# Optimization experiments

Measured on AMD Instinct MI355X. Metric: run time of the kernel, lower is better.

The kernel has to match this reference:

```python
import jax, jax.numpy as jnp
import numpy as np

T, B, I, H = 512, 256, 256, 256


def setup_inputs() -> dict:
    key = jax.random.key(0)
    ks = jax.random.split(key, 7)
    sk = 1.0 / np.sqrt(H)
    u = lambda k, shape: jax.random.uniform(k, shape, jnp.float32, -sk, sk)
    return {
        "x": jax.random.normal(ks[0], (T, B, I), jnp.float32),
        "W_ih": u(ks[1], (3 * H, I)),   # rows ordered [r, z, n] as in torch GRUCell
        "W_hh": u(ks[2], (3 * H, H)),
        "b_ih": u(ks[3], (3 * H,)),
        "b_hh": u(ks[4], (3 * H,)),
        "W_out": u(ks[5], (1, H)),
        "b_out": u(ks[6], (1,)),
    }


def _gru_forward(x, W_ih, W_hh, b_ih, b_hh):
    # Precompute input projections for all timesteps in one big GEMM: [T,B,3H]
    gi_all = jnp.einsum("tbi,gi->tbg", x, W_ih) + b_ih

    def step(h, gi):
        gh = h @ W_hh.T + b_hh                      # [B, 3H]
        i_r, i_z, i_n = jnp.split(gi, 3, axis=-1)
        h_r, h_z, h_n = jnp.split(gh, 3, axis=-1)
        r = jax.nn.sigmoid(i_r + h_r)
        z = jax.nn.sigmoid(i_z + h_z)
        n = jnp.tanh(i_n + r * h_n)
        h_new = (1.0 - z) * n + z * h
        return h_new, None

    h0 = jnp.zeros((x.shape[1], W_hh.shape[1]), x.dtype)
    h_final, _ = jax.lax.scan(step, h0, gi_all)
    return h_final


def reference(x, W_ih, W_hh, b_ih, b_hh, W_out, b_out):
    h = _gru_forward(x, W_ih, W_hh, b_ih, b_hh)
    return jax.nn.sigmoid(h @ W_out.T + b_out)      # [B, 1]
```

## Files before the change

### kernel.cpp

```cpp
#include <hip/hip_runtime.h>
#include <hip/hip_bf16.h>


#define TT 512
#define BB 256
#define II 256
#define HH 256

#define SRZ (-1.4426950408889634f)
#define SN  (2.8853900817779268f)

typedef __attribute__((ext_vector_type(8))) short short8;
typedef __attribute__((ext_vector_type(4))) float f32x4;

__device__ __forceinline__ unsigned short rne_bf16(float f) {
  union { float f; unsigned u; } v; v.f = f;
  unsigned r = v.u + 0x7FFFu + ((v.u >> 16) & 1u);
  return (unsigned short)(r >> 16);
}
__device__ __forceinline__ float bf2f(unsigned short b) {
  union { unsigned u; float f; } v; v.u = ((unsigned)b) << 16;
  return v.f;
}
__device__ __forceinline__ float blo(unsigned p) {
  union { unsigned u; float f; } v; v.u = p << 16; return v.f;
}
__device__ __forceinline__ float bhi(unsigned p) {
  union { unsigned u; float f; } v; v.u = p & 0xffff0000u; return v.f;
}
__device__ __forceinline__ float sigm(float x) { return 1.0f / (1.0f + __expf(-x)); }
__device__ __forceinline__ float tanhfast(float x) {
  return 1.0f - 2.0f / (__expf(2.0f * x) + 1.0f);
}

__device__ __forceinline__ short8 ldw8(const float* __restrict__ p) {
  float4 a = *reinterpret_cast<const float4*>(p);
  float4 b = *reinterpret_cast<const float4*>(p + 4);
  short8 r;
  r[0] = (short)rne_bf16(a.x); r[1] = (short)rne_bf16(a.y);
  r[2] = (short)rne_bf16(a.z); r[3] = (short)rne_bf16(a.w);
  r[4] = (short)rne_bf16(b.x); r[5] = (short)rne_bf16(b.y);
  r[6] = (short)rne_bf16(b.z); r[7] = (short)rne_bf16(b.w);
  return r;
}
__device__ __forceinline__ short8 ldw8s(const float* __restrict__ p, float s) {
  float4 a = *reinterpret_cast<const float4*>(p);
  float4 b = *reinterpret_cast<const float4*>(p + 4);
  short8 r;
  r[0] = (short)rne_bf16(a.x * s); r[1] = (short)rne_bf16(a.y * s);
  r[2] = (short)rne_bf16(a.z * s); r[3] = (short)rne_bf16(a.w * s);
  r[4] = (short)rne_bf16(b.x * s); r[5] = (short)rne_bf16(b.y * s);
  r[6] = (short)rne_bf16(b.z * s); r[7] = (short)rne_bf16(b.w * s);
  return r;
}

#define SWZ8(m, k) ((m) * 256 + ((k) ^ (((m) & 7) * 8)))
#define SWZ(m, k) ((m) * 256 + ((k) ^ ((m) * 16)))

__device__ __forceinline__ void pin_agpr(short8& w) {
  asm volatile("" : "+a"(w));
}
__device__ __forceinline__ void mfma_ag(f32x4& d, short8 a, const short8& b) {
  asm volatile("v_mfma_f32_16x16x32_bf16 %0, %1, %2, %0"
               : "+v"(d) : "v"(a), "a"(b));
}
__device__ __forceinline__ void mfma_ag_f(f32x4& d, short8 a, const short8& b) {
  asm volatile("s_nop 1\n\tv_mfma_f32_16x16x32_bf16 %0, %1, %2, %0"
               : "+v"(d) : "v"(a), "a"(b));
}
__device__ __forceinline__ void mfma_v(f32x4& d, short8 a, short8 b) {
  asm volatile("v_mfma_f32_16x16x32_bf16 %0, %1, %2, %0"
               : "+v"(d) : "v"(a), "v"(b));
}
__device__ __forceinline__ void mfma_v_f(f32x4& d, short8 a, short8 b) {
  asm volatile("s_nop 1\n\tv_mfma_f32_16x16x32_bf16 %0, %1, %2, %0"
               : "+v"(d) : "v"(a), "v"(b));
}
__device__ __forceinline__ void mfma_fence6(f32x4& a0, f32x4& a1, f32x4& a2,
                                            f32x4& a3, f32x4& a4, f32x4& a5) {
  asm volatile("s_nop 7\n\ts_nop 7"
               : "+v"(a0), "+v"(a1), "+v"(a2), "+v"(a3), "+v"(a4), "+v"(a5));
}
__device__ __forceinline__ unsigned cvtpk_bf16(float lo, float hi) {
  unsigned r;
  asm("v_cvt_pk_bf16_f32 %0, %1, %2" : "=v"(r) : "v"(lo), "v"(hi));
  return r;
}

__global__ __launch_bounds__(512)
__attribute__((amdgpu_waves_per_eu(2, 2)))
void gi_gemm8(const float* __restrict__ x, const float* __restrict__ Wih,
              const float* __restrict__ bih, const float* __restrict__ bhh,
              unsigned short* __restrict__ gi, int ntiles) {
  __shared__ __align__(16) unsigned short ax[2][4096];
  const int tid = threadIdx.x, l = tid & 63, w = tid >> 6;
  const int g4 = l >> 4, i15 = l & 15;

  short8 wf[3][2][8];
  float bs[3][2];
#pragma unroll
  for (int g = 0; g < 3; ++g)
#pragma unroll
    for (int ct = 0; ct < 2; ++ct) {
      int j = 32 * w + 16 * ct + i15;
      float s = (g == 2) ? SN : SRZ;
#pragma unroll
      for (int c = 0; c < 8; ++c)
        wf[g][ct][c] = ldw8s(Wih + (size_t)(g * 256 + j) * 256 + c * 32 + g4 * 8, s);
      bs[g][ct] = (g == 2) ? SN * bih[512 + j]
                           : SRZ * (bih[g * 256 + j] + bhh[g * 256 + j]);
    }

  auto stage = [&](int buf, int t) {
#pragma unroll
    for (int p = 0; p < 2; ++p) {
      int idx = p * 512 + tid;
      int m = idx >> 6, k0 = (idx & 63) << 2;
      float4 v = *reinterpret_cast<const float4*>(x + (size_t)t * 4096 + m * 256 + k0);
      ushort4 b;
      b.x = rne_bf16(v.x); b.y = rne_bf16(v.y);
      b.z = rne_bf16(v.z); b.w = rne_bf16(v.w);
      *reinterpret_cast<ushort4*>(&ax[buf][SWZ8(m, k0)]) = b;
    }
  };

  if (blockIdx.x >= ntiles) return;
  stage(0, blockIdx.x);
  int cur = 0;
  for (int tile = blockIdx.x; tile < ntiles; tile += 256) {
    __syncthreads();
    int tn = tile + 256;
    if (tn < ntiles) stage(cur ^ 1, tn);
    f32x4 aR[2] = {{0, 0, 0, 0}, {0, 0, 0, 0}};
    f32x4 aZ[2] = {{0, 0, 0, 0}, {0, 0, 0, 0}};
    f32x4 aN[2] = {{0, 0, 0, 0}, {0, 0, 0, 0}};
#pragma unroll
    for (int c = 0; c < 8; ++c) {
      short8 ah = *reinterpret_cast<const short8*>(&ax[cur][SWZ8(l & 15, c * 32 + g4 * 8)]);
#pragma unroll
      for (int ct = 0; ct < 2; ++ct) {
        if (c == 0) {
          mfma_v_f(aR[ct], ah, wf[0][ct][0]);
          mfma_v_f(aZ[ct], ah, wf[1][ct][0]);
          mfma_v_f(aN[ct], ah, wf[2][ct][0]);
        } else {
          mfma_v(aR[ct], ah, wf[0][ct][c]);
          mfma_v(aZ[ct], ah, wf[1][ct][c]);
          mfma_v(aN[ct], ah, wf[2][ct][c]);
        }
      }
    }
    mfma_fence6(aR[0], aR[1], aZ[0], aZ[1], aN[0], aN[1]);
    unsigned short* gp = gi + ((size_t)tile * 512 + (size_t)(w * 64 + l)) * 24;
    short8 oR, oZ, oN;
#pragma unroll
    for (int ct = 0; ct < 2; ++ct)
#pragma unroll
      for (int q = 0; q < 4; ++q) {
        oR[ct * 4 + q] = (short)rne_bf16(aR[ct][q] + bs[0][ct]);
        oZ[ct * 4 + q] = (short)rne_bf16(aZ[ct][q] + bs[1][ct]);
        oN[ct * 4 + q] = (short)rne_bf16(aN[ct][q] + bs[2][ct]);
      }
    *reinterpret_cast<short8*>(gp) = oR;
    *reinterpret_cast<short8*>(gp + 8) = oZ;
    *reinterpret_cast<short8*>(gp + 16) = oN;
    cur ^= 1;
  }
}

__global__ __launch_bounds__(512)
__attribute__((amdgpu_waves_per_eu(2, 2)))
void gru_step10(const float* __restrict__ Whh, const float* __restrict__ bhh,
                const float* __restrict__ Wout, const float* __restrict__ bout,
                const unsigned short* __restrict__ gi, float* __restrict__ hchk,
                float* __restrict__ out, int t0, int nt) {
  __shared__ __align__(16) unsigned char arena[147456];
  unsigned short* ldsn = (unsigned short*)arena;
  unsigned short* hbuf0 = (unsigned short*)(arena + 131072);
  unsigned short* hbuf1 = (unsigned short*)(arena + 139264);
  const int tid = threadIdx.x, l = tid & 63, w = tid >> 6;
  const int g4 = l >> 4, i15 = l & 15;
  const int bx = blockIdx.x, b0 = bx * 16;

  short8 wR[2][8], wZ[2][8];
#pragma unroll
  for (int ct = 0; ct < 2; ++ct) {
    int j = 32 * w + 16 * ct + i15;
#pragma unroll
    for (int c = 0; c < 8; ++c) {
      wR[ct][c] = ldw8s(Whh + (size_t)j * 256 + c * 32 + g4 * 8, SRZ);
      wZ[ct][c] = ldw8s(Whh + (size_t)(256 + j) * 256 + c * 32 + g4 * 8, SRZ);
      pin_agpr(wR[ct][c]);
      pin_agpr(wZ[ct][c]);
    }
  }
  asm volatile("s_nop 7\n\ts_nop 7" ::: "memory");

  float cn[2];
#pragma unroll
  for (int tl = 0; tl < 2; ++tl) {
    int j = 32 * w + 16 * tl + i15;
#pragma unroll
    for (int c = 0; c < 8; ++c) {
      short8 fn = ldw8s(Whh + (size_t)(512 + j) * 256 + c * 32 + g4 * 8, SN);
      *reinterpret_cast<short8*>(
          &ldsn[(size_t)(((w * 2 + tl) * 8 + c) * 64 + l) * 8]) = fn;
    }
    cn[tl] = SN * bhh[512 + j];
  }
  const unsigned short* nbase = ldsn + (size_t)l * 8 + (size_t)w * 8192;

  unsigned hp[2][2];
  if (t0 == 0) {
    hp[0][0] = hp[0][1] = hp[1][0] = hp[1][1] = 0;
    for (int i = tid; i < 4096; i += 512) hbuf0[i] = 0;
  } else {
#pragma unroll
    for (int ct = 0; ct < 2; ++ct) {
      int j = 32 * w + 16 * ct + i15;
      float v0 = hchk[(size_t)(b0 + 4 * g4 + 0) * 256 + j];
      float v1 = hchk[(size_t)(b0 + 4 * g4 + 1) * 256 + j];
      float v2 = hchk[(size_t)(b0 + 4 * g4 + 2) * 256 + j];
      float v3 = hchk[(size_t)(b0 + 4 * g4 + 3) * 256 + j];
      hp[ct][0] = cvtpk_bf16(v0, v1);
      hp[ct][1] = cvtpk_bf16(v2, v3);
      hbuf0[SWZ8(4 * g4 + 0, j)] = (unsigned short)hp[ct][0];
      hbuf0[SWZ8(4 * g4 + 1, j)] = (unsigned short)(hp[ct][0] >> 16);
      hbuf0[SWZ8(4 * g4 + 2, j)] = (unsigned short)hp[ct][1];
      hbuf0[SWZ8(4 * g4 + 3, j)] = (unsigned short)(hp[ct][1] >> 16);
    }
  }
  const unsigned short* gp = gi + ((size_t)(bx * 8 + w) * 64 + l) * 24;
  __syncthreads();

#pragma unroll 1
  for (int lt = 0; lt < nt; ++lt) {
    short8 gR = *reinterpret_cast<const short8*>(gp);
    short8 gZ = *reinterpret_cast<const short8*>(gp + 8);
    short8 gN = *reinterpret_cast<const short8*>(gp + 16);

    f32x4 aR[2] = {{0, 0, 0, 0}, {0, 0, 0, 0}};
    f32x4 aZ[2] = {{0, 0, 0, 0}, {0, 0, 0, 0}};
    f32x4 aN[2] = {{0, 0, 0, 0}, {0, 0, 0, 0}};
    const unsigned short* hb = (lt & 1) ? hbuf1 : hbuf0;
    unsigned short* hw = (lt & 1) ? hbuf0 : hbuf1;
#pragma unroll
    for (int c = 0; c < 8; ++c) {
      short8 ah = *reinterpret_cast<const short8*>(&hb[SWZ8(l & 15, c * 32 + g4 * 8)]);
      short8 fn0 = *reinterpret_cast<const short8*>(nbase + c * 512);
      short8 fn1 = *reinterpret_cast<const short8*>(nbase + (8 + c) * 512);
      if (c == 0) {
        mfma_ag_f(aR[0], ah, wR[0][0]);
        mfma_ag_f(aR[1], ah, wR[1][0]);
        mfma_ag_f(aZ[0], ah, wZ[0][0]);
        mfma_ag_f(aZ[1], ah, wZ[1][0]);
        mfma_v_f(aN[0], ah, fn0);
        mfma_v_f(aN[1], ah, fn1);
      } else {
        mfma_ag(aR[0], ah, wR[0][c]);
        mfma_ag(aR[1], ah, wR[1][c]);
        mfma_ag(aZ[0], ah, wZ[0][c]);
        mfma_ag(aZ[1], ah, wZ[1][c]);
        mfma_v(aN[0], ah, fn0);
        mfma_v(aN[1], ah, fn1);
      }
    }
    mfma_fence6(aR[0], aR[1], aZ[0], aZ[1], aN[0], aN[1]);

#pragma unroll
    for (int ct = 0; ct < 2; ++ct) {
      int j = 32 * w + 16 * ct + i15;
      float hq[4];
#pragma unroll
      for (int q = 0; q < 4; ++q) {
        float hold = (q & 1) ? bhi(hp[ct][q >> 1]) : blo(hp[ct][q >> 1]);
        float rr = __builtin_amdgcn_rcpf(
            1.0f + __builtin_amdgcn_exp2f(aR[ct][q] + bf2f((unsigned short)gR[ct * 4 + q])));
        float zz = __builtin_amdgcn_rcpf(
            1.0f + __builtin_amdgcn_exp2f(aZ[ct][q] + bf2f((unsigned short)gZ[ct * 4 + q])));
        float y = bf2f((unsigned short)gN[ct * 4 + q]) + rr * (aN[ct][q] + cn[ct]);
        float nn = 1.0f - 2.0f * __builtin_amdgcn_rcpf(1.0f + __builtin_amdgcn_exp2f(y));
        hq[q] = nn + zz * (hold - nn);
      }
      hp[ct][0] = cvtpk_bf16(hq[0], hq[1]);
      hp[ct][1] = cvtpk_bf16(hq[2], hq[3]);
      hw[SWZ8(4 * g4 + 0, j)] = (unsigned short)hp[ct][0];
      hw[SWZ8(4 * g4 + 1, j)] = (unsigned short)(hp[ct][0] >> 16);
      hw[SWZ8(4 * g4 + 2, j)] = (unsigned short)hp[ct][1];
      hw[SWZ8(4 * g4 + 3, j)] = (unsigned short)(hp[ct][1] >> 16);
    }
    gp += 196608;
    __syncthreads();
  }

  if (t0 + nt < TT) {
#pragma unroll
    for (int ct = 0; ct < 2; ++ct) {
      int j = 32 * w + 16 * ct + i15;
      hchk[(size_t)(b0 + 4 * g4 + 0) * 256 + j] = blo(hp[ct][0]);
      hchk[(size_t)(b0 + 4 * g4 + 1) * 256 + j] = bhi(hp[ct][0]);
      hchk[(size_t)(b0 + 4 * g4 + 2) * 256 + j] = blo(hp[ct][1]);
      hchk[(size_t)(b0 + 4 * g4 + 3) * 256 + j] = bhi(hp[ct][1]);
    }
  } else {
    float* hfin = (float*)arena;
#pragma unroll
    for (int ct = 0; ct < 2; ++ct) {
      int j = 32 * w + 16 * ct + i15;
      hfin[(4 * g4 + 0) * 256 + j] = blo(hp[ct][0]);
      hfin[(4 * g4 + 1) * 256 + j] = bhi(hp[ct][0]);
      hfin[(4 * g4 + 2) * 256 + j] = blo(hp[ct][1]);
      hfin[(4 * g4 + 3) * 256 + j] = bhi(hp[ct][1]);
    }
    __syncthreads();
#pragma unroll
    for (int rr = 0; rr < 2; ++rr) {
      int r = 2 * w + rr;
      float s = 0.0f;
#pragma unroll
      for (int k = 0; k < 4; ++k) {
        int col = l + 64 * k;
        s += hfin[r * 256 + col] * Wout[col];
      }
#pragma unroll
      for (int off = 32; off > 0; off >>= 1) s += __shfl_xor(s, off, 64);
      if (l == 0) out[b0 + r] = sigm(s + bout[0]);
    }
  }
}

__global__ __launch_bounds__(1024, 1) void gru_fused_legacy(
    const float* __restrict__ x, const float* __restrict__ Wih,
    const float* __restrict__ Whh, const float* __restrict__ bih,
    const float* __restrict__ bhh, const float* __restrict__ Wout,
    const float* __restrict__ bout, float* __restrict__ out) {
  __shared__ unsigned short hbuf[2][16 * 256];
  __shared__ unsigned short xbuf[2][16 * 256];
  __shared__ float hfin[16][256];
  int tid = threadIdx.x, lane = tid & 63, w = tid >> 6;
  int i15 = lane & 15, g4 = lane >> 4;
  int b0 = blockIdx.x * 16;
  int j = 16 * w + i15;

  short8 whh0[8], whh1[8], whh2[8], wih0[8], wih1[8], wih2[8];
#pragma unroll
  for (int c = 0; c < 8; ++c) {
    int ko = c * 32 + g4 * 8;
    whh0[c] = ldw8(Whh + (size_t)j * 256 + ko);
    whh1[c] = ldw8(Whh + (size_t)(256 + j) * 256 + ko);
    whh2[c] = ldw8(Whh + (size_t)(512 + j) * 256 + ko);
    wih0[c] = ldw8(Wih + (size_t)j * 256 + ko);
    wih1[c] = ldw8(Wih + (size_t)(256 + j) * 256 + ko);
    wih2[c] = ldw8(Wih + (size_t)(512 + j) * 256 + ko);
  }
  float bias_r = bih[j] + bhh[j];
  float bias_z = bih[256 + j] + bhh[256 + j];
  float bihn = bih[512 + j], bhhn = bhh[512 + j];

  f32x4 h = {0, 0, 0, 0};
  for (int idx = tid; idx < 16 * 256; idx += 1024) hbuf[0][idx] = 0;
  {
    int m = tid >> 6, k0 = (tid & 63) << 2;
    float4 v = *reinterpret_cast<const float4*>(x + (size_t)b0 * II + m * 256 + k0);
    ushort4 b;
    b.x = rne_bf16(v.x); b.y = rne_bf16(v.y);
    b.z = rne_bf16(v.z); b.w = rne_bf16(v.w);
    *reinterpret_cast<ushort4*>(&xbuf[0][SWZ(m, k0)]) = b;
  }
  __syncthreads();

  for (int lt = 0; lt < TT; ++lt) {
    int cur = lt & 1, nxt = cur ^ 1;
    short8 ah[8], axf[8];
#pragma unroll
    for (int c = 0; c < 8; ++c) {
      int m = lane & 15, k0 = c * 32 + g4 * 8;
      ah[c] = *reinterpret_cast<const short8*>(&hbuf[cur][SWZ(m, k0)]);
      axf[c] = *reinterpret_cast<const short8*>(&xbuf[cur][SWZ(m, k0)]);
    }
    f32x4 gr = {0, 0, 0, 0}, gz = {0, 0, 0, 0}, gn = {0, 0, 0, 0};
    f32x4 ar = {0, 0, 0, 0}, az = {0, 0, 0, 0}, an = {0, 0, 0, 0};
#pragma unroll
    for (int c = 0; c < 8; ++c) {
      gr = __builtin_amdgcn_mfma_f32_16x16x32_bf16(axf[c], wih0[c], gr, 0, 0, 0);
      gz = __builtin_amdgcn_mfma_f32_16x16x32_bf16(axf[c], wih1[c], gz, 0, 0, 0);
      gn = __builtin_amdgcn_mfma_f32_16x16x32_bf16(axf[c], wih2[c], gn, 0, 0, 0);
    }
    if (lt + 1 < TT) {
      int m = tid >> 6, k0 = (tid & 63) << 2;
      float4 v = *reinterpret_cast<const float4*>(
          x + ((size_t)(lt + 1) * BB + b0) * II + m * 256 + k0);
      ushort4 b;
      b.x = rne_bf16(v.x); b.y = rne_bf16(v.y);
      b.z = rne_bf16(v.z); b.w = rne_bf16(v.w);
      *reinterpret_cast<ushort4*>(&xbuf[nxt][SWZ(m, k0)]) = b;
    }
#pragma unroll
    for (int c = 0; c < 8; ++c) {
      ar = __builtin_amdgcn_mfma_f32_16x16x32_bf16(ah[c], whh0[c], ar, 0, 0, 0);
      az = __builtin_amdgcn_mfma_f32_16x16x32_bf16(ah[c], whh1[c], az, 0, 0, 0);
      an = __builtin_amdgcn_mfma_f32_16x16x32_bf16(ah[c], whh2[c], an, 0, 0, 0);
    }
#pragma unroll
    for (int q = 0; q < 4; ++q) {
      float r = sigm(ar[q] + gr[q] + bias_r);
      float zz = sigm(az[q] + gz[q] + bias_z);
      float nn = tanhfast(gn[q] + bihn + r * (an[q] + bhhn));
      float hq = (1.0f - zz) * nn + zz * h[q];
      h[q] = hq;
      hbuf[nxt][SWZ(g4 * 4 + q, j)] = rne_bf16(hq);
    }
    __syncthreads();
  }
#pragma unroll
  for (int q = 0; q < 4; ++q) hfin[g4 * 4 + q][j] = h[q];
  __syncthreads();
  float s = 0.0f;
#pragma unroll
  for (int i = 0; i < 4; ++i) {
    int k = lane + 64 * i;
    s += hfin[w][k] * Wout[k];
  }
#pragma unroll
  for (int off = 32; off > 0; off >>= 1) s += __shfl_xor(s, off, 64);
  if (lane == 0) out[b0 + w] = sigm(s + bout[0]);
}

extern "C" void kernel_launch(void* const* d_in, const int* in_sizes, int n_in,
                              void* d_out, int out_size, void* d_ws, size_t ws_size,
                              hipStream_t stream) {
  const float* x    = (const float*)d_in[0];
  const float* Wih  = (const float*)d_in[1];
  const float* Whh  = (const float*)d_in[2];
  const float* bih  = (const float*)d_in[3];
  const float* bhh  = (const float*)d_in[4];
  const float* Wout = (const float*)d_in[5];
  const float* bout = (const float*)d_in[6];
  float* out = (float*)d_out;

  const size_t HBYTES = (size_t)BB * HH * sizeof(float);
  const size_t STEP_BYTES = (size_t)16 * 512 * 48;
  size_t gi_cap = ws_size > HBYTES ? ws_size - HBYTES : 0;
  long tc = (long)(gi_cap / STEP_BYTES);
  if (tc > TT) tc = TT;

  if (tc >= 32) {
    float* hchk = (float*)d_ws;
    unsigned short* gi = (unsigned short*)((char*)d_ws + HBYTES);
    for (int t0 = 0; t0 < TT; t0 += (int)tc) {
      int nt = (TT - t0) < (int)tc ? (TT - t0) : (int)tc;
      gi_gemm8<<<dim3(256), dim3(512), 0, stream>>>(
          x + (size_t)t0 * BB * II, Wih, bih, bhh, gi, nt * 16);
      gru_step10<<<dim3(16), dim3(512), 0, stream>>>(
          Whh, bhh, Wout, bout, gi, hchk, out, t0, nt);
    }
  } else {
    gru_fused_legacy<<<dim3(16), dim3(1024), 0, stream>>>(
        x, Wih, Whh, bih, bhh, Wout, bout, out);
  }
}
```

Baseline: 924.7 us.

## Split GRU recurrence across 32 blocks of 8 batch rows each

The recurrent step kernel now handles 8 batch rows per block instead of 16 and launches 32 workgroups, so the serial recurrence is spread over twice as many compute units. The MFMA still computes a padded 16-row tile whose upper half is zeroed. Lanes use ds_bpermute to pick the accumulator column that belongs to their own row/column slot, which halves the per-lane elementwise gate work. The gi GEMM epilogue writes a matching 12-element record layout. In exchange, half of each MFMA is wasted, extra permute instructions are added, and the weights are loaded into twice as many blocks.

```diff
diff --git a/kernel.cpp b/kernel.cpp
--- a/kernel.cpp
+++ b/kernel.cpp
@@ -86,12 +86,17 @@
   asm("v_cvt_pk_bf16_f32 %0, %1, %2" : "=v"(r) : "v"(lo), "v"(hi));
   return r;
 }
+__device__ __forceinline__ float bperm_sel(int paddr, bool hi, float a0, float a1) {
+  int p0 = __builtin_amdgcn_ds_bpermute(paddr, __builtin_bit_cast(int, a0));
+  int p1 = __builtin_amdgcn_ds_bpermute(paddr, __builtin_bit_cast(int, a1));
+  return __builtin_bit_cast(float, hi ? p1 : p0);
+}
 
 __global__ __launch_bounds__(512)
 __attribute__((amdgpu_waves_per_eu(2, 2)))
-void gi_gemm8(const float* __restrict__ x, const float* __restrict__ Wih,
-              const float* __restrict__ bih, const float* __restrict__ bhh,
-              unsigned short* __restrict__ gi, int ntiles) {
+void gi_gemm12(const float* __restrict__ x, const float* __restrict__ Wih,
+               const float* __restrict__ bih, const float* __restrict__ bhh,
+               unsigned short* __restrict__ gi, int ntiles) {
   __shared__ __align__(16) unsigned short ax[2][4096];
   const int tid = threadIdx.x, l = tid & 63, w = tid >> 6;
   const int g4 = l >> 4, i15 = l & 15;
@@ -151,26 +156,31 @@
       }
     }
     mfma_fence6(aR[0], aR[1], aZ[0], aZ[1], aN[0], aN[1]);
-    unsigned short* gp = gi + ((size_t)tile * 512 + (size_t)(w * 64 + l)) * 24;
-    short8 oR, oZ, oN;
-#pragma unroll
-    for (int ct = 0; ct < 2; ++ct)
-#pragma unroll
-      for (int q = 0; q < 4; ++q) {
-        oR[ct * 4 + q] = (short)rne_bf16(aR[ct][q] + bs[0][ct]);
-        oZ[ct * 4 + q] = (short)rne_bf16(aZ[ct][q] + bs[1][ct]);
-        oN[ct * 4 + q] = (short)rne_bf16(aN[ct][q] + bs[2][ct]);
-      }
-    *reinterpret_cast<short8*>(gp) = oR;
-    *reinterpret_cast<short8*>(gp + 8) = oZ;
-    *reinterpret_cast<short8*>(gp + 16) = oN;
+
+    int tloc = tile >> 4, btile = tile & 15;
+    size_t recbase = ((size_t)(tloc * 32 + 2 * btile + (g4 >> 1)) * 512 +
+                      (size_t)w * 64 + (size_t)((g4 & 1) * 32)) * 12;
+#pragma unroll
+    for (int ct = 0; ct < 2; ++ct) {
+      size_t rec = recbase + (size_t)(16 * ct + i15) * 12;
+      ushort4 oR, oZ, oN;
+      oR.x = rne_bf16(aR[ct][0] + bs[0][ct]); oR.y = rne_bf16(aR[ct][1] + bs[0][ct]);
+      oR.z = rne_bf16(aR[ct][2] + bs[0][ct]); oR.w = rne_bf16(aR[ct][3] + bs[0][ct]);
+      oZ.x = rne_bf16(aZ[ct][0] + bs[1][ct]); oZ.y = rne_bf16(aZ[ct][1] + bs[1][ct]);
+      oZ.z = rne_bf16(aZ[ct][2] + bs[1][ct]); oZ.w = rne_bf16(aZ[ct][3] + bs[1][ct]);
+      oN.x = rne_bf16(aN[ct][0] + bs[2][ct]); oN.y = rne_bf16(aN[ct][1] + bs[2][ct]);
+      oN.z = rne_bf16(aN[ct][2] + bs[2][ct]); oN.w = rne_bf16(aN[ct][3] + bs[2][ct]);
+      *reinterpret_cast<ushort4*>(gi + rec) = oR;
+      *reinterpret_cast<ushort4*>(gi + rec + 4) = oZ;
+      *reinterpret_cast<ushort4*>(gi + rec + 8) = oN;
+    }
     cur ^= 1;
   }
 }
 
 __global__ __launch_bounds__(512)
 __attribute__((amdgpu_waves_per_eu(2, 2)))
-void gru_step10(const float* __restrict__ Whh, const float* __restrict__ bhh,
+void gru_step12(const float* __restrict__ Whh, const float* __restrict__ bhh,
                 const float* __restrict__ Wout, const float* __restrict__ bout,
                 const unsigned short* __restrict__ gi, float* __restrict__ hchk,
                 float* __restrict__ out, int t0, int nt) {
@@ -180,7 +190,11 @@
   unsigned short* hbuf1 = (unsigned short*)(arena + 139264);
   const int tid = threadIdx.x, l = tid & 63, w = tid >> 6;
   const int g4 = l >> 4, i15 = l & 15;
-  const int bx = blockIdx.x, b0 = bx * 16;
+  const int bx = blockIdx.x, b0 = bx * 8;
+  const int colL = 32 * w + (l & 31);
+  const int rbase = 4 * (l >> 5);
+  const int paddr = ((((l >> 5) << 4) | (l & 15)) << 2);
+  const bool ctHi = (l & 16) != 0;
 
   short8 wR[2][8], wZ[2][8];
 #pragma unroll
@@ -196,7 +210,6 @@
   }
   asm volatile("s_nop 7\n\ts_nop 7" ::: "memory");
 
-  float cn[2];
 #pragma unroll
   for (int tl = 0; tl < 2; ++tl) {
     int j = 32 * w + 16 * tl + i15;
@@ -206,38 +219,39 @@
       *reinterpret_cast<short8*>(
           &ldsn[(size_t)(((w * 2 + tl) * 8 + c) * 64 + l) * 8]) = fn;
     }
-    cn[tl] = SN * bhh[512 + j];
   }
   const unsigned short* nbase = ldsn + (size_t)l * 8 + (size_t)w * 8192;
-
-  unsigned hp[2][2];
+  const float cn = SN * bhh[512 + colL];
+
+  unsigned hp[2];
+  {
+    int idx = 2048 + tid;
+    hbuf0[idx] = 0; hbuf0[idx + 512] = 0; hbuf0[idx + 1024] = 0; hbuf0[idx + 1536] = 0;
+    hbuf1[idx] = 0; hbuf1[idx + 512] = 0; hbuf1[idx + 1024] = 0; hbuf1[idx + 1536] = 0;
+  }
   if (t0 == 0) {
-    hp[0][0] = hp[0][1] = hp[1][0] = hp[1][1] = 0;
-    for (int i = tid; i < 4096; i += 512) hbuf0[i] = 0;
+    hp[0] = 0; hp[1] = 0;
+    for (int i = tid; i < 2048; i += 512) hbuf0[i] = 0;
   } else {
-#pragma unroll
-    for (int ct = 0; ct < 2; ++ct) {
-      int j = 32 * w + 16 * ct + i15;
-      float v0 = hchk[(size_t)(b0 + 4 * g4 + 0) * 256 + j];
-      float v1 = hchk[(size_t)(b0 + 4 * g4 + 1) * 256 + j];
-      float v2 = hchk[(size_t)(b0 + 4 * g4 + 2) * 256 + j];
-      float v3 = hchk[(size_t)(b0 + 4 * g4 + 3) * 256 + j];
-      hp[ct][0] = cvtpk_bf16(v0, v1);
-      hp[ct][1] = cvtpk_bf16(v2, v3);
-      hbuf0[SWZ8(4 * g4 + 0, j)] = (unsigned short)hp[ct][0];
-      hbuf0[SWZ8(4 * g4 + 1, j)] = (unsigned short)(hp[ct][0] >> 16);
-      hbuf0[SWZ8(4 * g4 + 2, j)] = (unsigned short)hp[ct][1];
-      hbuf0[SWZ8(4 * g4 + 3, j)] = (unsigned short)(hp[ct][1] >> 16);
-    }
-  }
-  const unsigned short* gp = gi + ((size_t)(bx * 8 + w) * 64 + l) * 24;
+    float v0 = hchk[(size_t)(b0 + rbase + 0) * 256 + colL];
+    float v1 = hchk[(size_t)(b0 + rbase + 1) * 256 + colL];
+    float v2 = hchk[(size_t)(b0 + rbase + 2) * 256 + colL];
+    float v3 = hchk[(size_t)(b0 + rbase + 3) * 256 + colL];
+    hp[0] = cvtpk_bf16(v0, v1);
+    hp[1] = cvtpk_bf16(v2, v3);
+    hbuf0[SWZ8(rbase + 0, colL)] = (unsigned short)hp[0];
+    hbuf0[SWZ8(rbase + 1, colL)] = (unsigned short)(hp[0] >> 16);
+    hbuf0[SWZ8(rbase + 2, colL)] = (unsigned short)hp[1];
+    hbuf0[SWZ8(rbase + 3, colL)] = (unsigned short)(hp[1] >> 16);
+  }
+  const unsigned short* gp = gi + ((size_t)bx * 512 + (size_t)(w * 64 + l)) * 12;
   __syncthreads();
 
 #pragma unroll 1
   for (int lt = 0; lt < nt; ++lt) {
-    short8 gR = *reinterpret_cast<const short8*>(gp);
-    short8 gZ = *reinterpret_cast<const short8*>(gp + 8);
-    short8 gN = *reinterpret_cast<const short8*>(gp + 16);
+    ushort4 gR = *reinterpret_cast<const ushort4*>(gp);
+    ushort4 gZ = *reinterpret_cast<const ushort4*>(gp + 4);
+    ushort4 gN = *reinterpret_cast<const ushort4*>(gp + 8);
 
     f32x4 aR[2] = {{0, 0, 0, 0}, {0, 0, 0, 0}};
     f32x4 aZ[2] = {{0, 0, 0, 0}, {0, 0, 0, 0}};
@@ -267,65 +281,61 @@
     }
     mfma_fence6(aR[0], aR[1], aZ[0], aZ[1], aN[0], aN[1]);
 
-#pragma unroll
-    for (int ct = 0; ct < 2; ++ct) {
-      int j = 32 * w + 16 * ct + i15;
-      float hq[4];
-#pragma unroll
-      for (int q = 0; q < 4; ++q) {
-        float hold = (q & 1) ? bhi(hp[ct][q >> 1]) : blo(hp[ct][q >> 1]);
-        float rr = __builtin_amdgcn_rcpf(
-            1.0f + __builtin_amdgcn_exp2f(aR[ct][q] + bf2f((unsigned short)gR[ct * 4 + q])));
-        float zz = __builtin_amdgcn_rcpf(
-            1.0f + __builtin_amdgcn_exp2f(aZ[ct][q] + bf2f((unsigned short)gZ[ct * 4 + q])));
-        float y = bf2f((unsigned short)gN[ct * 4 + q]) + rr * (aN[ct][q] + cn[ct]);
-        float nn = 1.0f - 2.0f * __builtin_amdgcn_rcpf(1.0f + __builtin_amdgcn_exp2f(y));
-        hq[q] = nn + zz * (hold - nn);
-      }
-      hp[ct][0] = cvtpk_bf16(hq[0], hq[1]);
-      hp[ct][1] = cvtpk_bf16(hq[2], hq[3]);
-      hw[SWZ8(4 * g4 + 0, j)] = (unsigned short)hp[ct][0];
-      hw[SWZ8(4 * g4 + 1, j)] = (unsigned short)(hp[ct][0] >> 16);
-      hw[SWZ8(4 * g4 + 2, j)] = (unsigned short)hp[ct][1];
-      hw[SWZ8(4 * g4 + 3, j)] = (unsigned short)(hp[ct][1] >> 16);
-    }
+    float vR[4], vZ[4], vN[4];
+#pragma unroll
+    for (int q = 0; q < 4; ++q) {
+      vR[q] = bperm_sel(paddr, ctHi, aR[0][q], aR[1][q]);
+      vZ[q] = bperm_sel(paddr, ctHi, aZ[0][q], aZ[1][q]);
+      vN[q] = bperm_sel(paddr, ctHi, aN[0][q], aN[1][q]);
+    }
+
+    float hq[4];
+    const unsigned short* gRp = (const unsigned short*)&gR;
+    const unsigned short* gZp = (const unsigned short*)&gZ;
+    const unsigned short* gNp = (const unsigned short*)&gN;
+#pragma unroll
+    for (int q = 0; q < 4; ++q) {
+      float hold = (q & 1) ? bhi(hp[q >> 1]) : blo(hp[q >> 1]);
+      float rr = __builtin_amdgcn_rcpf(
+          1.0f + __builtin_amdgcn_exp2f(vR[q] + bf2f(gRp[q])));
+      float zz = __builtin_amdgcn_rcpf(
+          1.0f + __builtin_amdgcn_exp2f(vZ[q] + bf2f(gZp[q])));
+      float y = bf2f(gNp[q]) + rr * (vN[q] + cn);
+      float nn = 1.0f - 2.0f * __builtin_amdgcn_rcpf(1.0f + __builtin_amdgcn_exp2f(y));
+      hq[q] = nn + zz * (hold - nn);
+    }
+    hp[0] = cvtpk_bf16(hq[0], hq[1]);
+    hp[1] = cvtpk_bf16(hq[2], hq[3]);
+    hw[SWZ8(rbase + 0, colL)] = (unsigned short)hp[0];
+    hw[SWZ8(rbase + 1, colL)] = (unsigned short)(hp[0] >> 16);
+    hw[SWZ8(rbase + 2, colL)] = (unsigned short)hp[1];
+    hw[SWZ8(rbase + 3, colL)] = (unsigned short)(hp[1] >> 16);
     gp += 196608;
     __syncthreads();
   }
 
   if (t0 + nt < TT) {
-#pragma unroll
-    for (int ct = 0; ct < 2; ++ct) {
-      int j = 32 * w + 16 * ct + i15;
-      hchk[(size_t)(b0 + 4 * g4 + 0) * 256 + j] = blo(hp[ct][0]);
-      hchk[(size_t)(b0 + 4 * g4 + 1) * 256 + j] = bhi(hp[ct][0]);
-      hchk[(size_t)(b0 + 4 * g4 + 2) * 256 + j] = blo(hp[ct][1]);
-      hchk[(size_t)(b0 + 4 * g4 + 3) * 256 + j] = bhi(hp[ct][1]);
-    }
+    hchk[(size_t)(b0 + rbase + 0) * 256 + colL] = blo(hp[0]);
+    hchk[(size_t)(b0 + rbase + 1) * 256 + colL] = bhi(hp[0]);
+    hchk[(size_t)(b0 + rbase + 2) * 256 + colL] = blo(hp[1]);
+    hchk[(size_t)(b0 + rbase + 3) * 256 + colL] = bhi(hp[1]);
   } else {
     float* hfin = (float*)arena;
-#pragma unroll
-    for (int ct = 0; ct < 2; ++ct) {
-      int j = 32 * w + 16 * ct + i15;
-      hfin[(4 * g4 + 0) * 256 + j] = blo(hp[ct][0]);
-      hfin[(4 * g4 + 1) * 256 + j] = bhi(hp[ct][0]);
-      hfin[(4 * g4 + 2) * 256 + j] = blo(hp[ct][1]);
-      hfin[(4 * g4 + 3) * 256 + j] = bhi(hp[ct][1]);
-    }
     __syncthreads();
-#pragma unroll
-    for (int rr = 0; rr < 2; ++rr) {
-      int r = 2 * w + rr;
-      float s = 0.0f;
-#pragma unroll
-      for (int k = 0; k < 4; ++k) {
-        int col = l + 64 * k;
-        s += hfin[r * 256 + col] * Wout[col];
-      }
-#pragma unroll
-      for (int off = 32; off > 0; off >>= 1) s += __shfl_xor(s, off, 64);
-      if (l == 0) out[b0 + r] = sigm(s + bout[0]);
-    }
+    hfin[(rbase + 0) * 256 + colL] = blo(hp[0]);
+    hfin[(rbase + 1) * 256 + colL] = bhi(hp[0]);
+    hfin[(rbase + 2) * 256 + colL] = blo(hp[1]);
+    hfin[(rbase + 3) * 256 + colL] = bhi(hp[1]);
+    __syncthreads();
+    float s = 0.0f;
+#pragma unroll
+    for (int k = 0; k < 4; ++k) {
+      int col = l + 64 * k;
+      s += hfin[w * 256 + col] * Wout[col];
+    }
+#pragma unroll
+    for (int off = 32; off > 0; off >>= 1) s += __shfl_xor(s, off, 64);
+    if (l == 0) out[b0 + w] = sigm(s + bout[0]);
   }
 }
 
@@ -439,7 +449,7 @@
   float* out = (float*)d_out;
 
   const size_t HBYTES = (size_t)BB * HH * sizeof(float);
-  const size_t STEP_BYTES = (size_t)16 * 512 * 48;
+  const size_t STEP_BYTES = (size_t)32 * 512 * 24;
   size_t gi_cap = ws_size > HBYTES ? ws_size - HBYTES : 0;
   long tc = (long)(gi_cap / STEP_BYTES);
   if (tc > TT) tc = TT;
@@ -449,9 +459,9 @@
     unsigned short* gi = (unsigned short*)((char*)d_ws + HBYTES);
     for (int t0 = 0; t0 < TT; t0 += (int)tc) {
       int nt = (TT - t0) < (int)tc ? (TT - t0) : (int)tc;
-      gi_gemm8<<<dim3(256), dim3(512), 0, stream>>>(
+      gi_gemm12<<<dim3(256), dim3(512), 0, stream>>>(
           x + (size_t)t0 * BB * II, Wih, bih, bhh, gi, nt * 16);
-      gru_step10<<<dim3(16), dim3(512), 0, stream>>>(
+      gru_step12<<<dim3(32), dim3(512), 0, stream>>>(
           Whh, bhh, Wout, bout, gi, hchk, out, t0, nt);
     }
   } else {
```

Measured after the change: 977.2 us. 1.06x slower.
